# Performance work log

Measured on AMD Instinct MI355X. Metric: run time of the kernel, lower is better.

## Reference

```python
import jax, jax.numpy as jnp
import numpy as np

T = 1.0  # temperature from __init__ (t=1)


def setup_inputs() -> dict:
    key = jax.random.key(0)
    k1, k2, k3 = jax.random.split(key, 3)
    N, C, D = 262144, 1024, 128
    feats = jax.random.normal(k1, (N, D), dtype=jnp.float32)
    prototypes = jax.random.normal(k2, (C, D), dtype=jnp.float32)
    labels = jax.random.randint(k3, (N,), 0, C, dtype=jnp.int64)
    return {"feats": feats, "prototypes": prototypes, "labels": labels}


def _dce_loss(feats, prototypes, labels):
    # same math as sqrt(sum((x[:,None,:]-y)**2, -1)) without the NxCxD tensor.
    x_sq = jnp.sum(feats * feats, axis=-1, keepdims=True)          # [N,1]
    y_sq = jnp.sum(prototypes * prototypes, axis=-1)               # [C]
    xy = jnp.einsum('nd,cd->nc', feats, prototypes)                # [N,C]
    sq_dist = jnp.maximum(x_sq + y_sq[None, :] - 2.0 * xy, 0.0)
    logits = -jnp.sqrt(sq_dist) / T                                # [N,C]
    logp = jax.nn.log_softmax(logits, axis=-1)
    nll = -jnp.take_along_axis(logp, labels[:, None], axis=-1)[:, 0]
    return jnp.mean(nll)  # CrossEntropyLoss default reduction='mean'


def reference(feats, prototypes, labels):
    return _dce_loss(feats, prototypes, labels)
```

## Files before the change

kernel.cpp:

```cpp
#include <hip/hip_runtime.h>
#include <hip/hip_bf16.h>

typedef __bf16 bf16x8 __attribute__((ext_vector_type(8)));
typedef __bf16 bf16x2 __attribute__((ext_vector_type(2)));
typedef float f32x4 __attribute__((ext_vector_type(4)));

#define K2f 2.0813689810056077f
#define LN2f 0.6931471805599453f

__global__ void dce_prep(const float* __restrict__ protos,
                         unsigned short* __restrict__ bpf,
                         float* __restrict__ ysq2) {
    int c = blockIdx.x;
    int lane = threadIdx.x;
    float2 f = ((const float2*)(protos))[c * 64 + lane];
    int d0 = lane * 2;
    int kk = d0 >> 5, sub = d0 & 31, lg = sub >> 3, e = sub & 7;
    size_t o = (((size_t)((c >> 4) * 4 + kk) * 64) + lg * 16 + (c & 15)) * 8 + e;
    bf16x2 h;
    h.x = (__bf16)f.x;
    h.y = (__bf16)f.y;
    *(bf16x2*)(bpf + o) = h;
    float xs = f.x * f.x + f.y * f.y;
#pragma unroll
    for (int d = 1; d < 64; d <<= 1) xs += __shfl_xor(xs, d);
    if (lane == 0) ysq2[c] = xs * K2f;
}

__global__ __launch_bounds__(256, 4) void dce_main(
    const float* __restrict__ feats,
    const float* __restrict__ protos,
    const unsigned short* __restrict__ bpf,
    const float* __restrict__ ysq2,
    const int* __restrict__ labels,
    float* __restrict__ partials, int C) {
    const int tid = threadIdx.x;
    const int lane = tid & 63;
    const int w = tid >> 6;
    const int row0 = blockIdx.x * 256;
    const int rbase = row0 + w * 64;
    const int lr = lane & 15;
    const int lg = lane >> 4;

    const int lab = labels[row0 + tid];
    const float4* fx = (const float4*)(feats + (size_t)(row0 + tid) * 128);
    const float4* px = (const float4*)(protos + (size_t)lab * 128);
    float xx = 0.f, yy = 0.f, xy = 0.f;
#pragma unroll 8
    for (int i = 0; i < 32; ++i) {
        float4 f = fx[i], p = px[i];
        xx = fmaf(f.x, f.x, fmaf(f.y, f.y, fmaf(f.z, f.z, fmaf(f.w, f.w, xx))));
        yy = fmaf(p.x, p.x, fmaf(p.y, p.y, fmaf(p.z, p.z, fmaf(p.w, p.w, yy))));
        xy = fmaf(f.x, p.x, fmaf(f.y, p.y, fmaf(f.z, p.z, fmaf(f.w, p.w, xy))));
    }
    const float ld = __builtin_amdgcn_sqrtf(fmaxf(fmaf(-2.f, xy, xx + yy), 0.f));

    bf16x8 a[4][4];
    const float4* f4 = (const float4*)feats;
#pragma unroll
    for (int m = 0; m < 4; ++m) {
        int r = rbase + m * 16 + lr;
#pragma unroll
        for (int kk = 0; kk < 4; ++kk) {
            int idx = r * 32 + kk * 8 + lg * 2;
            float4 lo = f4[idx];
            float4 hi = f4[idx + 1];
            bf16x8 v;
            v[0] = (__bf16)lo.x; v[1] = (__bf16)lo.y; v[2] = (__bf16)lo.z; v[3] = (__bf16)lo.w;
            v[4] = (__bf16)hi.x; v[5] = (__bf16)hi.y; v[6] = (__bf16)hi.z; v[7] = (__bf16)hi.w;
            a[m][kk] = v;
        }
    }

    float xsqs[4][4];
#pragma unroll
    for (int m = 0; m < 4; ++m)
#pragma unroll
        for (int reg = 0; reg < 4; ++reg)
            xsqs[m][reg] = K2f * __shfl(xx, m * 16 + lg * 4 + reg);

    float lacc[4][4];
#pragma unroll
    for (int m = 0; m < 4; ++m)
#pragma unroll
        for (int reg = 0; reg < 4; ++reg) lacc[m][reg] = 0.f;

    const bf16x8* bv = (const bf16x8*)bpf;
    const int nt = C >> 4;
    for (int ct = 0; ct < nt; ++ct) {
        bf16x8 b[4];
#pragma unroll
        for (int kk = 0; kk < 4; ++kk) b[kk] = bv[(ct * 4 + kk) * 64 + lane];
        const float yq2 = ysq2[ct * 16 + lr];
#pragma unroll
        for (int m = 0; m < 4; ++m) {
            f32x4 acc = {0.f, 0.f, 0.f, 0.f};
#pragma unroll
            for (int kk = 0; kk < 4; ++kk)
                acc = __builtin_amdgcn_mfma_f32_16x16x32_bf16(a[m][kk], b[kk], acc, 0, 0, 0);
#pragma unroll
            for (int reg = 0; reg < 4; ++reg) {
                float d = fmaf(-2.f * K2f, acc[reg], xsqs[m][reg] + yq2);
                d = fmaxf(d, 0.f);
                float s = __builtin_amdgcn_sqrtf(d);
                lacc[m][reg] += __builtin_amdgcn_exp2f(-s);
            }
        }
    }

    float ssum = 0.f;
#pragma unroll
    for (int m = 0; m < 4; ++m)
#pragma unroll
        for (int reg = 0; reg < 4; ++reg) {
            float l = lacc[m][reg];
            l += __shfl_xor(l, 1);
            l += __shfl_xor(l, 2);
            l += __shfl_xor(l, 4);
            l += __shfl_xor(l, 8);
            float ldv = __shfl(ld, m * 16 + lg * 4 + reg);
            if (lr == 0) ssum += ldv + LN2f * __builtin_amdgcn_logf(l);
        }
    ssum += __shfl_xor(ssum, 16);
    ssum += __shfl_xor(ssum, 32);

    __shared__ float red[4];
    if (lane == 0) red[w] = ssum;
    __syncthreads();
    if (tid == 0) partials[blockIdx.x] = red[0] + red[1] + red[2] + red[3];
}

__global__ void dce_finish(const float* __restrict__ partials,
                           float* __restrict__ out, int nblocks, float invN) {
    int tid = threadIdx.x;
    float s = 0.f;
    for (int i = tid; i < nblocks; i += 256) s += partials[i];
#pragma unroll
    for (int d = 1; d < 64; d <<= 1) s += __shfl_xor(s, d);
    __shared__ float red[4];
    if ((tid & 63) == 0) red[tid >> 6] = s;
    __syncthreads();
    if (tid == 0) out[0] = (red[0] + red[1] + red[2] + red[3]) * invN;
}

extern "C" void kernel_launch(void* const* d_in, const int* in_sizes, int n_in,
                              void* d_out, int out_size, void* d_ws, size_t ws_size,
                              hipStream_t stream) {
    const float* feats = (const float*)d_in[0];
    const float* protos = (const float*)d_in[1];
    const int* labels = (const int*)d_in[2];
    const int N = in_sizes[2];
    const int C = in_sizes[1] / 128;
    float* out = (float*)d_out;

    unsigned short* bpf = (unsigned short*)d_ws;
    float* ysq2 = (float*)((char*)d_ws + (size_t)C * 128 * 2);
    float* partials = ysq2 + C;
    const int nblocks = N / 256;

    dce_prep<<<C, 64, 0, stream>>>(protos, bpf, ysq2);
    dce_main<<<nblocks, 256, 0, stream>>>(feats, protos, bpf, ysq2, labels, partials, C);
    dce_finish<<<1, 256, 0, stream>>>(partials, out, nblocks, 1.0f / (float)N);
}
```

Measured before the change: 141.3 us.

## Stage prototype tiles in LDS via async global_load_lds, halve rows per block

Each block now handles 128 rows, with each wave covering 32 rows, so the grid doubles. The label-distance prologue is split across two threads per row and combined with a shuffle. Prototype B fragments are no longer read by every wave straight from global memory. They are double-buffered into shared memory with global_load_lds and shared across the four waves, which cuts L2 traffic for B. The cost is a __syncthreads per tile, and half as much MFMA work is amortized per B load per wave.

```diff
diff --git a/kernel.cpp b/kernel.cpp
--- a/kernel.cpp
+++ b/kernel.cpp
@@ -7,6 +7,13 @@
 
 #define K2f 2.0813689810056077f
 #define LN2f 0.6931471805599453f
+
+typedef __attribute__((address_space(3))) unsigned int lds_u32;
+typedef __attribute__((address_space(1))) unsigned int glb_u32;
+
+__device__ __forceinline__ void gload16(const void* g, void* l) {
+    __builtin_amdgcn_global_load_lds((const glb_u32*)g, (lds_u32*)l, 16, 0, 0);
+}
 
 __global__ void dce_prep(const float* __restrict__ protos,
                          unsigned short* __restrict__ bpf,
@@ -37,32 +44,40 @@
     const int tid = threadIdx.x;
     const int lane = tid & 63;
     const int w = tid >> 6;
-    const int row0 = blockIdx.x * 256;
-    const int rbase = row0 + w * 64;
+    const int row0 = blockIdx.x * 128;
+    const int rbase = row0 + w * 32;
     const int lr = lane & 15;
     const int lg = lane >> 4;
 
-    const int lab = labels[row0 + tid];
-    const float4* fx = (const float4*)(feats + (size_t)(row0 + tid) * 128);
-    const float4* px = (const float4*)(protos + (size_t)lab * 128);
+    __shared__ __align__(16) unsigned char bsm[2][4096];
+    __shared__ float red[4];
+
+    const int r1 = row0 + (tid >> 1);
+    const int half = tid & 1;
+    const int lab = labels[r1];
+    const float4* fx = (const float4*)feats + (size_t)r1 * 32 + half * 16;
+    const float4* px = (const float4*)protos + (size_t)lab * 32 + half * 16;
     float xx = 0.f, yy = 0.f, xy = 0.f;
-#pragma unroll 8
-    for (int i = 0; i < 32; ++i) {
+#pragma unroll
+    for (int i = 0; i < 16; ++i) {
         float4 f = fx[i], p = px[i];
         xx = fmaf(f.x, f.x, fmaf(f.y, f.y, fmaf(f.z, f.z, fmaf(f.w, f.w, xx))));
         yy = fmaf(p.x, p.x, fmaf(p.y, p.y, fmaf(p.z, p.z, fmaf(p.w, p.w, yy))));
         xy = fmaf(f.x, p.x, fmaf(f.y, p.y, fmaf(f.z, p.z, fmaf(f.w, p.w, xy))));
     }
+    xx += __shfl_xor(xx, 1);
+    yy += __shfl_xor(yy, 1);
+    xy += __shfl_xor(xy, 1);
     const float ld = __builtin_amdgcn_sqrtf(fmaxf(fmaf(-2.f, xy, xx + yy), 0.f));
 
-    bf16x8 a[4][4];
+    bf16x8 a[2][4];
     const float4* f4 = (const float4*)feats;
 #pragma unroll
-    for (int m = 0; m < 4; ++m) {
-        int r = rbase + m * 16 + lr;
+    for (int m = 0; m < 2; ++m) {
+        size_t r = (size_t)(rbase + m * 16 + lr);
 #pragma unroll
         for (int kk = 0; kk < 4; ++kk) {
-            int idx = r * 32 + kk * 8 + lg * 2;
+            size_t idx = r * 32 + kk * 8 + lg * 2;
             float4 lo = f4[idx];
             float4 hi = f4[idx + 1];
             bf16x8 v;
@@ -72,32 +87,40 @@
         }
     }
 
-    float xsqs[4][4];
+    float xsqs[2][4];
 #pragma unroll
-    for (int m = 0; m < 4; ++m)
+    for (int m = 0; m < 2; ++m)
 #pragma unroll
         for (int reg = 0; reg < 4; ++reg)
-            xsqs[m][reg] = K2f * __shfl(xx, m * 16 + lg * 4 + reg);
+            xsqs[m][reg] = K2f * __shfl(xx, 2 * (m * 16 + lg * 4 + reg));
 
-    float lacc[4][4];
+    float lacc[2][4];
 #pragma unroll
-    for (int m = 0; m < 4; ++m)
+    for (int m = 0; m < 2; ++m)
 #pragma unroll
         for (int reg = 0; reg < 4; ++reg) lacc[m][reg] = 0.f;
 
-    const bf16x8* bv = (const bf16x8*)bpf;
+    const char* bpc = (const char*)bpf;
     const int nt = C >> 4;
-    for (int ct = 0; ct < nt; ++ct) {
-        bf16x8 b[4];
+    gload16(bpc + (size_t)tid * 16, &bsm[0][tid * 16]);
+    int p = 0;
+    for (int t = 0; t < nt; ++t) {
+        __syncthreads();
+        if (t + 1 < nt)
+            gload16(bpc + (size_t)(t + 1) * 4096 + tid * 16, &bsm[p ^ 1][tid * 16]);
+        const bf16x8* bl = (const bf16x8*)&bsm[p][0];
+        bf16x8 b0 = bl[lane];
+        bf16x8 b1 = bl[64 + lane];
+        bf16x8 b2 = bl[128 + lane];
+        bf16x8 b3 = bl[192 + lane];
+        const float yq2 = ysq2[t * 16 + lr];
 #pragma unroll
-        for (int kk = 0; kk < 4; ++kk) b[kk] = bv[(ct * 4 + kk) * 64 + lane];
-        const float yq2 = ysq2[ct * 16 + lr];
-#pragma unroll
-        for (int m = 0; m < 4; ++m) {
+        for (int m = 0; m < 2; ++m) {
             f32x4 acc = {0.f, 0.f, 0.f, 0.f};
-#pragma unroll
-            for (int kk = 0; kk < 4; ++kk)
-                acc = __builtin_amdgcn_mfma_f32_16x16x32_bf16(a[m][kk], b[kk], acc, 0, 0, 0);
+            acc = __builtin_amdgcn_mfma_f32_16x16x32_bf16(a[m][0], b0, acc, 0, 0, 0);
+            acc = __builtin_amdgcn_mfma_f32_16x16x32_bf16(a[m][1], b1, acc, 0, 0, 0);
+            acc = __builtin_amdgcn_mfma_f32_16x16x32_bf16(a[m][2], b2, acc, 0, 0, 0);
+            acc = __builtin_amdgcn_mfma_f32_16x16x32_bf16(a[m][3], b3, acc, 0, 0, 0);
 #pragma unroll
             for (int reg = 0; reg < 4; ++reg) {
                 float d = fmaf(-2.f * K2f, acc[reg], xsqs[m][reg] + yq2);
@@ -106,11 +129,12 @@
                 lacc[m][reg] += __builtin_amdgcn_exp2f(-s);
             }
         }
+        p ^= 1;
     }
 
     float ssum = 0.f;
 #pragma unroll
-    for (int m = 0; m < 4; ++m)
+    for (int m = 0; m < 2; ++m)
 #pragma unroll
         for (int reg = 0; reg < 4; ++reg) {
             float l = lacc[m][reg];
@@ -118,13 +142,12 @@
             l += __shfl_xor(l, 2);
             l += __shfl_xor(l, 4);
             l += __shfl_xor(l, 8);
-            float ldv = __shfl(ld, m * 16 + lg * 4 + reg);
+            float ldv = __shfl(ld, 2 * (m * 16 + lg * 4 + reg));
             if (lr == 0) ssum += ldv + LN2f * __builtin_amdgcn_logf(l);
         }
     ssum += __shfl_xor(ssum, 16);
     ssum += __shfl_xor(ssum, 32);
 
-    __shared__ float red[4];
     if (lane == 0) red[w] = ssum;
     __syncthreads();
     if (tid == 0) partials[blockIdx.x] = red[0] + red[1] + red[2] + red[3];
@@ -156,7 +179,7 @@
     unsigned short* bpf = (unsigned short*)d_ws;
     float* ysq2 = (float*)((char*)d_ws + (size_t)C * 128 * 2);
     float* partials = ysq2 + C;
-    const int nblocks = N / 256;
+    const int nblocks = N / 128;
 
     dce_prep<<<C, 64, 0, stream>>>(protos, bpf, ysq2);
     dce_main<<<nblocks, 256, 0, stream>>>(feats, protos, bpf, ysq2, labels, partials, C);
```

Measured after the change: 161.2 us. 14.0% more time.
